# Kernel tuning notes

Hardware: AMD Instinct MI355X
Metric: run time of the kernel (lower is better)

## Reference

```python
import jax, jax.numpy as jnp
import numpy as np

N_HEADS = 4  # from init_kwargs


def setup_inputs() -> dict:
    rng = jax.random.key(0)
    ks = jax.random.split(rng, 7)
    S, B, D = 512, 16, 2048  # seqlen must equal head_dim (D // N_HEADS) per module's reshape
    w_scale = 0.02  # keep logits in a sane range so softmax is not one-hot
    return {
        "query": jax.random.normal(ks[0], (S, B, D), dtype=jnp.float32),
        "key": jax.random.normal(ks[1], (S, B, D), dtype=jnp.float32),
        "value": jax.random.normal(ks[2], (S, B, D), dtype=jnp.float32),
        "Wq": jax.random.normal(ks[3], (D, D), dtype=jnp.float32) * w_scale,
        "Wk": jax.random.normal(ks[4], (D, D), dtype=jnp.float32) * w_scale,
        "Wv": jax.random.normal(ks[5], (D, D), dtype=jnp.float32) * w_scale,
        "Wo": jax.random.normal(ks[6], (D, D), dtype=jnp.float32) * w_scale,
    }


def reference(query, key, value, Wq, Wk, Wv, Wo):
    # Dropout layers act as identity (inference mode). RoPE helper exists in the
    # original module but is never invoked in forward(), so it is omitted.
    S, B, D = query.shape
    H = N_HEADS
    hd = D // H  # head_dim; note S == hd is required by the original reshapes

    def split_heads(x, W):
        # torch Linear: x @ W.T ; then (S,B,D)->(S,B,H,hd)->(H,B,S,hd)->(H*B,S,hd)
        y = x @ W.T
        return y.reshape(S, B, H, hd).transpose(2, 1, 0, 3).reshape(H * B, S, hd)

    q = split_heads(query, Wq)
    k = split_heads(key, Wk)
    v = split_heads(value, Wv)

    scores = jnp.einsum("nsd,ntd->nst", q, k) / jnp.sqrt(jnp.float32(hd))
    attn = jax.nn.softmax(scores, axis=-1)          # (H*B, S, S)
    out = jnp.einsum("nst,ntd->nsd", attn, v)        # (H*B, S, hd)

    # output: (H*B,S,hd)->(H,B,S,hd)->permute(1,2,0,3)->(B,S,H,hd)
    out4 = out.reshape(H, B, S, hd).transpose(1, 2, 0, 3)
    # attn_score reshape relies on S == hd, faithfully reproduced
    attn_score = attn.reshape(H, B, S, hd).transpose(1, 2, 0, 3)  # (B,S,H,hd)

    # .transpose(1,2).contiguous().view(S,B,-1): row-major reinterpret of (B,H,S,hd)
    out4 = jnp.swapaxes(out4, 1, 2)  # (B,H,S,hd)
    output = out4.reshape(S, B, D)

    output = output @ Wo.T
    return output, attn_score
```

## Files before the change

kernel.cpp:

```cpp
#include <hip/hip_runtime.h>
#include <hip/hip_bf16.h>
#include <math.h>

using bf16 = __hip_bfloat16;
typedef __attribute__((ext_vector_type(4))) float f32x4;
typedef __attribute__((ext_vector_type(8))) short s16x8;

#define BM 256
#define BN 256
#define BK 32
#define SLOT 16384
#define BREG 8192

__device__ __forceinline__ short f2b(float f) {
  bf16 h = __float2bfloat16(f);
  short s; __builtin_memcpy(&s, &h, 2); return s;
}

__device__ __forceinline__ void async16(const bf16* g, bf16* l) {
  __builtin_amdgcn_global_load_lds(
      (const __attribute__((address_space(1))) void*)g,
      (__attribute__((address_space(3))) void*)l, 16, 0, 0);
}

__device__ __forceinline__ f32x4 vmax4(f32x4 a, f32x4 b) {
  f32x4 r;
#pragma unroll
  for (int j = 0; j < 4; j++) r[j] = fmaxf(a[j], b[j]);
  return r;
}

template<int MODE, bool CF32>
__global__ __launch_bounds__(512, 2) void gemm_nt(const bf16* __restrict__ Ain,
    const bf16* __restrict__ Bin, void* __restrict__ Cout,
    int K, int lda, int ldb, int ldc, float alpha)
{
  __shared__ bf16 lds[4 * SLOT];

  const int tid  = threadIdx.x;
  const int lane = tid & 63;
  const int wave = tid >> 6;
  const int quad = lane >> 4;
  const int l16  = lane & 15;

  const int nwg = gridDim.x * gridDim.y * gridDim.z;
  int bid = (blockIdx.z * gridDim.y + blockIdx.y) * gridDim.x + blockIdx.x;
  bid = (bid & 7) * (nwg >> 3) + (bid >> 3);
  const int bx = bid % gridDim.x;
  int rest = bid / gridDim.x;
  const int by = rest % gridDim.y;
  const int bz = rest / gridDim.y;

  size_t aBase = 0, bBase = 0, cBase = 0;
  if (MODE == 2) {
    aBase = (size_t)(bz & 15) * 1048576 + (size_t)(bz >> 4) * 512;
    bBase = (size_t)bz * 262144;
    cBase = (size_t)((bz & 15) * 4 + (bz >> 4)) * 262144;
  }

  const int tileM = by * BM;
  const int tileN = bx * BN;

  const int sRow = tid >> 2;
  const int sQ   = (tid & 3) ^ ((tid >> 3) & 3);
  const int sCol = sQ * 8;
  const size_t aOff0 = aBase + (size_t)(tileM + sRow) * lda + sCol;
  const size_t aOff1 = aOff0 + (size_t)128 * lda;
  const size_t bOff0 = bBase + (size_t)(tileN + sRow) * ldb + sCol;
  const size_t bOff1 = bOff0 + (size_t)128 * ldb;
  const int t8 = tid * 8;

  const int warpRow = (wave >> 2) * 128;
  const int warpCol = (wave & 3) * 64;
  int offA[8], offB[4];
#pragma unroll
  for (int mi = 0; mi < 8; mi++) {
    const int R = warpRow + mi * 16 + l16;
    offA[mi] = R * 32 + ((quad ^ ((R >> 1) & 3)) * 8);
  }
#pragma unroll
  for (int ni = 0; ni < 4; ni++) {
    const int R = warpCol + ni * 16 + l16;
    offB[ni] = BREG + R * 32 + ((quad ^ ((R >> 1) & 3)) * 8);
  }

  f32x4 acc[8][4] = {};
  const int NT = K / BK;

#pragma unroll
  for (int p = 0; p < 3; ++p) {
    bf16* base = lds + p * SLOT;
    const int ks = p * BK;
    async16(Ain + aOff0 + ks, base + t8);
    async16(Ain + aOff1 + ks, base + 4096 + t8);
    async16(Bin + bOff0 + ks, base + BREG + t8);
    async16(Bin + bOff1 + ks, base + BREG + 4096 + t8);
  }
  asm volatile("s_waitcnt vmcnt(8)" ::: "memory");
  __builtin_amdgcn_s_barrier();

  for (int g = 0; g < NT; ++g) {
    if (g + 3 < NT) {
      bf16* base = lds + ((g + 3) & 3) * SLOT;
      const int ks = (g + 3) * BK;
      async16(Ain + aOff0 + ks, base + t8);
      async16(Ain + aOff1 + ks, base + 4096 + t8);
      async16(Bin + bOff0 + ks, base + BREG + t8);
      async16(Bin + bOff1 + ks, base + BREG + 4096 + t8);
    }

    const bf16* lb = lds + (g & 3) * SLOT;
    s16x8 af[8], bfr[4];
#pragma unroll
    for (int mi = 0; mi < 8; mi++) af[mi] = *(const s16x8*)(lb + offA[mi]);
#pragma unroll
    for (int ni = 0; ni < 4; ni++) bfr[ni] = *(const s16x8*)(lb + offB[ni]);

    __builtin_amdgcn_s_setprio(1);
#pragma unroll
    for (int mi = 0; mi < 8; mi++)
#pragma unroll
      for (int ni = 0; ni < 4; ni++)
        acc[mi][ni] = __builtin_amdgcn_mfma_f32_16x16x32_bf16(af[mi], bfr[ni], acc[mi][ni], 0, 0, 0);
    __builtin_amdgcn_s_setprio(0);

    if (g < NT - 1) {
      const int ahead = (g + 3 < NT ? 2 : (g + 2 < NT ? NT - 2 - g : 0));
      if (ahead == 2)      asm volatile("s_waitcnt vmcnt(8)" ::: "memory");
      else if (ahead == 1) asm volatile("s_waitcnt vmcnt(4)" ::: "memory");
      else                 asm volatile("s_waitcnt vmcnt(0)" ::: "memory");
      __builtin_amdgcn_s_barrier();
    }
  }

#pragma unroll
  for (int mi = 0; mi < 8; mi++) {
#pragma unroll
    for (int ni = 0; ni < 4; ni++) {
      f32x4 v = acc[mi][ni];
      const int col = tileN + warpCol + ni * 16 + l16;
#pragma unroll
      for (int r = 0; r < 4; r++) {
        const int row = tileM + warpRow + mi * 16 + quad * 4 + r;
        const float val = v[r] * alpha;
        size_t dst;
        if (MODE == 0) {
          dst = (((size_t)((col >> 9) * 16 + (row & 15)) * 512 + (size_t)(row >> 4)) * 512)
                + (size_t)(col & 511);
        } else {
          dst = cBase + (size_t)row * ldc + (size_t)col;
        }
        if (CF32) ((float*)Cout)[dst] = val;
        else      ((bf16*)Cout)[dst] = __float2bfloat16(val);
      }
    }
  }
}

#define SSLOT 20480
__global__ __launch_bounds__(512, 2) void scores_softmax(
    const bf16* __restrict__ Q, const bf16* __restrict__ Kh,
    float* __restrict__ P, bf16* __restrict__ Pb, float alpha)
{
  __shared__ bf16 lds[3 * SSLOT];

  const int tid  = threadIdx.x;
  const int lane = tid & 63;
  const int wave = tid >> 6;
  const int quad = lane >> 4;
  const int l16  = lane & 15;

  int bid = blockIdx.z * 4 + blockIdx.y;
  bid = (bid & 7) * 32 + (bid >> 3);
  const int by = bid & 3;
  const int bz = bid >> 2;

  const size_t aBase = (size_t)bz * 262144;
  const size_t bBase = (size_t)bz * 262144;
  const size_t cBase = (size_t)(bz & 15) * 1048576 + (size_t)(bz >> 4) * 512;
  const int tileM = by * 128;

  const int sRow = tid >> 2;
  const int sQz  = (tid & 3) ^ ((tid >> 3) & 3);
  const int sCol = sQz * 8;
  const size_t aOff = aBase + (size_t)(tileM + sRow) * 512 + sCol;
  const size_t bOff = bBase + (size_t)sRow * 512 + sCol;
  const int t8 = tid * 8;

  const int warpRow = (wave >> 2) * 64;
  const int warpCol = (wave & 3) * 128;
  int offA[4], offB[8];
#pragma unroll
  for (int mi = 0; mi < 4; mi++) {
    const int R = warpRow + mi * 16 + l16;
    offA[mi] = R * 32 + ((quad ^ ((R >> 1) & 3)) * 8);
  }
#pragma unroll
  for (int ni = 0; ni < 8; ni++) {
    const int R = warpCol + ni * 16 + l16;
    offB[ni] = 4096 + R * 32 + ((quad ^ ((R >> 1) & 3)) * 8);
  }

  f32x4 acc[4][8] = {};

#pragma unroll
  for (int p = 0; p < 2; ++p) {
    bf16* base = lds + p * SSLOT;
    const int ks = p * BK;
    async16(Q + aOff + ks, base + t8);
#pragma unroll
    for (int c = 0; c < 4; c++)
      async16(Kh + bOff + c * 65536 + ks, base + 4096 + c * 4096 + t8);
  }
  asm volatile("s_waitcnt vmcnt(5)" ::: "memory");
  __builtin_amdgcn_s_barrier();

  for (int g = 0; g < 16; ++g) {
    if (g + 2 < 16) {
      bf16* base = lds + ((g + 2) % 3) * SSLOT;
      const int ks = (g + 2) * BK;
      async16(Q + aOff + ks, base + t8);
#pragma unroll
      for (int c = 0; c < 4; c++)
        async16(Kh + bOff + c * 65536 + ks, base + 4096 + c * 4096 + t8);
    }

    const bf16* lb = lds + (g % 3) * SSLOT;
    s16x8 af[4], bfr[8];
#pragma unroll
    for (int mi = 0; mi < 4; mi++) af[mi] = *(const s16x8*)(lb + offA[mi]);
#pragma unroll
    for (int ni = 0; ni < 8; ni++) bfr[ni] = *(const s16x8*)(lb + offB[ni]);

    __builtin_amdgcn_s_setprio(1);
#pragma unroll
    for (int mi = 0; mi < 4; mi++)
#pragma unroll
      for (int ni = 0; ni < 8; ni++)
        acc[mi][ni] = __builtin_amdgcn_mfma_f32_16x16x32_bf16(af[mi], bfr[ni], acc[mi][ni], 0, 0, 0);
    __builtin_amdgcn_s_setprio(0);

    if (g + 2 < 16) {
      asm volatile("s_waitcnt vmcnt(5)" ::: "memory");
      __builtin_amdgcn_s_barrier();
    } else if (g + 1 < 16) {
      asm volatile("s_waitcnt vmcnt(0)" ::: "memory");
      __builtin_amdgcn_s_barrier();
    }
  }

  __syncthreads();
  float* red  = (float*)lds;
  float* red2 = red + 512;
  const int wv = wave & 3;

#pragma unroll
  for (int mi = 0; mi < 4; mi++)
#pragma unroll
    for (int ni = 0; ni < 8; ni++) acc[mi][ni] *= alpha;

  f32x4 gm[4];
#pragma unroll
  for (int mi = 0; mi < 4; mi++) {
    f32x4 mx = acc[mi][0];
#pragma unroll
    for (int ni = 1; ni < 8; ni++) mx = vmax4(mx, acc[mi][ni]);
#pragma unroll
    for (int off = 1; off <= 8; off <<= 1) {
      f32x4 o;
#pragma unroll
      for (int r = 0; r < 4; r++) o[r] = __shfl_xor(mx[r], off, 64);
      mx = vmax4(mx, o);
    }
    if (l16 == 0) {
      const int rw = warpRow + mi * 16 + quad * 4;
#pragma unroll
      for (int r = 0; r < 4; r++) red[(rw + r) * 4 + wv] = mx[r];
    }
  }
  __syncthreads();
#pragma unroll
  for (int mi = 0; mi < 4; mi++) {
    const int rw = warpRow + mi * 16 + quad * 4;
#pragma unroll
    for (int r = 0; r < 4; r++) {
      f32x4 p = *(const f32x4*)&red[(rw + r) * 4];
      gm[mi][r] = fmaxf(fmaxf(p[0], p[1]), fmaxf(p[2], p[3]));
    }
  }
  f32x4 sm[4] = {};
#pragma unroll
  for (int mi = 0; mi < 4; mi++)
#pragma unroll
    for (int ni = 0; ni < 8; ni++) {
      f32x4 v = acc[mi][ni];
#pragma unroll
      for (int r = 0; r < 4; r++) v[r] = __expf(v[r] - gm[mi][r]);
      acc[mi][ni] = v;
      sm[mi] += v;
    }
#pragma unroll
  for (int mi = 0; mi < 4; mi++) {
#pragma unroll
    for (int off = 1; off <= 8; off <<= 1) {
      f32x4 o;
#pragma unroll
      for (int r = 0; r < 4; r++) o[r] = __shfl_xor(sm[mi][r], off, 64);
      sm[mi] += o;
    }
    if (l16 == 0) {
      const int rw = warpRow + mi * 16 + quad * 4;
#pragma unroll
      for (int r = 0; r < 4; r++) red2[(rw + r) * 4 + wv] = sm[mi][r];
    }
  }
  __syncthreads();
#pragma unroll
  for (int mi = 0; mi < 4; mi++) {
    const int rw = warpRow + mi * 16 + quad * 4;
#pragma unroll
    for (int r = 0; r < 4; r++) {
      f32x4 p = *(const f32x4*)&red2[(rw + r) * 4];
      gm[mi][r] = 1.f / (p[0] + p[1] + p[2] + p[3]);
    }
  }
#pragma unroll
  for (int mi = 0; mi < 4; mi++)
#pragma unroll
    for (int ni = 0; ni < 8; ni++) {
      const int col = warpCol + ni * 16 + l16;
#pragma unroll
      for (int r = 0; r < 4; r++) {
        const int row = tileM + warpRow + mi * 16 + quad * 4 + r;
        const size_t idx = cBase + (size_t)row * 2048 + col;
        const float val = acc[mi][ni][r] * gm[mi][r];
        P[idx]  = val;
        Pb[idx] = __float2bfloat16(val);
      }
    }
}

struct Conv6 {
  const float* src[6];
  bf16* dst[6];
  int n[6];
};

__global__ __launch_bounds__(256) void convert6(Conv6 a) {
  const int t = blockIdx.y;
  const float* __restrict__ src = a.src[t];
  bf16* __restrict__ dst = a.dst[t];
  const size_t n = (size_t)a.n[t];
  const size_t stride = (size_t)gridDim.x * 256 * 64;
  for (size_t i = ((size_t)blockIdx.x * 256 + threadIdx.x) * 64; i < n; i += stride) {
    f32x4 x[16];
#pragma unroll
    for (int j = 0; j < 16; j++) x[j] = *(const f32x4*)(src + i + j * 4);
    s16x8 r[8];
#pragma unroll
    for (int j = 0; j < 8; j++) {
#pragma unroll
      for (int k = 0; k < 4; k++) {
        r[j][k]     = f2b(x[2 * j][k]);
        r[j][4 + k] = f2b(x[2 * j + 1][k]);
      }
    }
#pragma unroll
    for (int j = 0; j < 8; j++) *(s16x8*)(dst + i + j * 8) = r[j];
  }
}

__global__ __launch_bounds__(256) void transpose512(const bf16* __restrict__ V,
                                                    bf16* __restrict__ VT) {
  __shared__ bf16 tile[32][33];
  const int n = blockIdx.z;
  const bf16* src = V + (size_t)n * 262144;
  bf16* dst = VT + (size_t)n * 262144;
  const int x = blockIdx.x * 32 + threadIdx.x;
#pragma unroll
  for (int i = 0; i < 32; i += 8)
    tile[threadIdx.y + i][threadIdx.x] =
        src[(size_t)(blockIdx.y * 32 + threadIdx.y + i) * 512 + x];
  __syncthreads();
  const int tcol = blockIdx.y * 32 + threadIdx.x;
#pragma unroll
  for (int i = 0; i < 32; i += 8)
    dst[(size_t)(blockIdx.x * 32 + threadIdx.y + i) * 512 + tcol] =
        tile[threadIdx.x][threadIdx.y + i];
}

extern "C" void kernel_launch(void* const* d_in, const int* in_sizes, int n_in,
                              void* d_out, int out_size, void* d_ws, size_t ws_size,
                              hipStream_t stream) {
  const float* query = (const float*)d_in[0];
  const float* key   = (const float*)d_in[1];
  const float* value = (const float*)d_in[2];
  const float* Wq = (const float*)d_in[3];
  const float* Wk = (const float*)d_in[4];
  const float* Wv = (const float*)d_in[5];
  const float* Wo = (const float*)d_in[6];
  float* out = (float*)d_out;
  float* P   = out + 16777216;

  bf16* ws0 = (bf16*)d_ws;
  bf16* ws1 = ws0 + 16777216;
  bf16* o0  = (bf16*)d_out;
  bf16* o1  = o0 + 16777216;
  bf16* p0  = (bf16*)P;
  bf16* p1  = p0 + 16777216;

  const dim3 blk(256);
  const dim3 gblk(512);
  const float inv_sqrt_hd = 0.04419417382415922f;

  Conv6 c;
  c.src[0] = query; c.dst[0] = ws0;           c.n[0] = 16777216;
  c.src[1] = key;   c.dst[1] = ws1;           c.n[1] = 16777216;
  c.src[2] = value; c.dst[2] = p0;            c.n[2] = 16777216;
  c.src[3] = Wq;    c.dst[3] = p1;            c.n[3] = 4194304;
  c.src[4] = Wk;    c.dst[4] = p1 + 4194304;  c.n[4] = 4194304;
  c.src[5] = Wv;    c.dst[5] = p1 + 8388608;  c.n[5] = 4194304;
  convert6<<<dim3(1024, 6), blk, 0, stream>>>(c);

  gemm_nt<0, false><<<dim3(8, 32, 1), gblk, 0, stream>>>(ws0, p1,           o0,  2048, 2048, 2048, 0, 1.0f);
  gemm_nt<0, false><<<dim3(8, 32, 1), gblk, 0, stream>>>(ws1, p1 + 4194304, o1,  2048, 2048, 2048, 0, 1.0f);
  gemm_nt<0, false><<<dim3(8, 32, 1), gblk, 0, stream>>>(p0,  p1 + 8388608, ws0, 2048, 2048, 2048, 0, 1.0f);

  scores_softmax<<<dim3(1, 4, 64), gblk, 0, stream>>>(o0, o1, P, ws1, inv_sqrt_hd);

  transpose512<<<dim3(16, 16, 64), dim3(32, 8), 0, stream>>>(ws0, o0);

  gemm_nt<2, false><<<dim3(2, 2, 64), gblk, 0, stream>>>(ws1, o0, ws0, 512, 2048, 512, 512, 1.0f);

  Conv6 cw;
  for (int i = 0; i < 6; i++) { cw.src[i] = Wo; cw.dst[i] = ws1; cw.n[i] = 4194304; }
  convert6<<<dim3(256, 1), blk, 0, stream>>>(cw);

  gemm_nt<3, true><<<dim3(8, 32, 1), gblk, 0, stream>>>(ws0, ws1, out, 2048, 2048, 2048, 2048, 1.0f);
}
```

Baseline: 711.0 us.

## Rewrite GEMM as 8-wave quadrant-pipelined kernel with BK=64 double buffer

Replaces the 4-stage BK=32 GEMM main loop with a two-slot BK=64 double-buffered scheme. Each wave computes four 64x32 quadrant sub-tiles, and LDS reads, async global-to-LDS staging and MFMA bursts are interleaved with barriers between each quadrant. The aim is to overlap memory traffic with matrix-core work more finely and to cut per-iteration loop overhead. The convert kernel is also changed to a strided coalesced access pattern with an occupancy hint. The many barriers and the tighter waitcnt scheduling risk stalls if the ordering is not balanced.

```diff
diff --git a/kernel.cpp b/kernel.cpp
--- a/kernel.cpp
+++ b/kernel.cpp
@@ -5,12 +5,6 @@
 using bf16 = __hip_bfloat16;
 typedef __attribute__((ext_vector_type(4))) float f32x4;
 typedef __attribute__((ext_vector_type(8))) short s16x8;
-
-#define BM 256
-#define BN 256
-#define BK 32
-#define SLOT 16384
-#define BREG 8192
 
 __device__ __forceinline__ short f2b(float f) {
   bf16 h = __float2bfloat16(f);
@@ -30,12 +24,62 @@
   return r;
 }
 
+#define BAR __builtin_amdgcn_s_barrier()
+#define VM6 asm volatile("s_waitcnt vmcnt(6)" ::: "memory")
+#define VM0 asm volatile("s_waitcnt vmcnt(0)" ::: "memory")
+
+#define STG_A(S, h, tile) do { \
+  const bf16* g_ = aS0 + (size_t)((h) * 128) * lda + (size_t)(tile) * 64; \
+  bf16* d_ = lds + (S) * 32768 + (h) * 8192 + stD; \
+  async16(g_, d_); async16(g_ + (size_t)64 * lda, d_ + 4096); } while (0)
+
+#define STG_B(S, h, tile) do { \
+  const bf16* g_ = bS0 + (size_t)((h) * 128) * ldb + (size_t)(tile) * 64; \
+  bf16* d_ = lds + (S) * 32768 + 16384 + (h) * 8192 + stD; \
+  async16(g_, d_); async16(g_ + (size_t)64 * ldb, d_ + 4096); } while (0)
+
+#define RD_A(S, qm) do { \
+  const bf16* pa0_ = lds + (S) * 32768 + (qm) * 8192 + rdA0; \
+  const bf16* pa1_ = lds + (S) * 32768 + (qm) * 8192 + rdA1; \
+  _Pragma("unroll") for (int mi = 0; mi < 4; mi++) { \
+    af[mi * 2]     = *(const s16x8*)(pa0_ + mi * 1024); \
+    af[mi * 2 + 1] = *(const s16x8*)(pa1_ + mi * 1024); } } while (0)
+
+#define RD_B(S, qn, B) do { \
+  const bf16* pb0_ = lds + (S) * 32768 + 16384 + (qn) * 8192 + rdB0; \
+  const bf16* pb1_ = lds + (S) * 32768 + 16384 + (qn) * 8192 + rdB1; \
+  _Pragma("unroll") for (int ni = 0; ni < 2; ni++) { \
+    B[ni * 2]     = *(const s16x8*)(pb0_ + ni * 1024); \
+    B[ni * 2 + 1] = *(const s16x8*)(pb1_ + ni * 1024); } } while (0)
+
+#define MM(qm, qn, B) do { \
+  __builtin_amdgcn_s_setprio(1); \
+  _Pragma("unroll") for (int mi = 0; mi < 4; mi++) \
+  _Pragma("unroll") for (int ni = 0; ni < 2; ni++) { \
+    acc[qm][qn][mi][ni] = __builtin_amdgcn_mfma_f32_16x16x32_bf16(af[mi*2],   B[ni*2],   acc[qm][qn][mi][ni], 0, 0, 0); \
+    acc[qm][qn][mi][ni] = __builtin_amdgcn_mfma_f32_16x16x32_bf16(af[mi*2+1], B[ni*2+1], acc[qm][qn][mi][ni], 0, 0, 0); } \
+  __builtin_amdgcn_s_setprio(0); } while (0)
+
+#define GROUP(S, OS, st1, stAll, tO, tN) do { \
+  RD_A(S, 0); RD_B(S, 0, bf0); \
+  if (st1) STG_A(OS, 1, tO); \
+  BAR; MM(0, 0, bf0); BAR; \
+  RD_B(S, 1, bf1); \
+  if (stAll) STG_A(S, 0, tN); \
+  BAR; MM(0, 1, bf1); BAR; \
+  RD_A(S, 1); \
+  if (stAll) STG_B(S, 0, tN); \
+  BAR; MM(1, 1, bf1); BAR; \
+  if (stAll) { STG_B(S, 1, tN); VM6; } else { VM0; } \
+  BAR; MM(1, 0, bf0); BAR; \
+} while (0)
+
 template<int MODE, bool CF32>
-__global__ __launch_bounds__(512, 2) void gemm_nt(const bf16* __restrict__ Ain,
+__global__ __launch_bounds__(512, 2) void gemm8(const bf16* __restrict__ Ain,
     const bf16* __restrict__ Bin, void* __restrict__ Cout,
     int K, int lda, int ldb, int ldc, float alpha)
 {
-  __shared__ bf16 lds[4 * SLOT];
+  __shared__ bf16 lds[2 * 32768];
 
   const int tid  = threadIdx.x;
   const int lane = tid & 63;
@@ -58,105 +102,74 @@
     cBase = (size_t)((bz & 15) * 4 + (bz >> 4)) * 262144;
   }
 
-  const int tileM = by * BM;
-  const int tileN = bx * BN;
-
-  const int sRow = tid >> 2;
-  const int sQ   = (tid & 3) ^ ((tid >> 3) & 3);
-  const int sCol = sQ * 8;
-  const size_t aOff0 = aBase + (size_t)(tileM + sRow) * lda + sCol;
-  const size_t aOff1 = aOff0 + (size_t)128 * lda;
-  const size_t bOff0 = bBase + (size_t)(tileN + sRow) * ldb + sCol;
-  const size_t bOff1 = bOff0 + (size_t)128 * ldb;
-  const int t8 = tid * 8;
-
-  const int warpRow = (wave >> 2) * 128;
-  const int warpCol = (wave & 3) * 64;
-  int offA[8], offB[4];
-#pragma unroll
-  for (int mi = 0; mi < 8; mi++) {
-    const int R = warpRow + mi * 16 + l16;
-    offA[mi] = R * 32 + ((quad ^ ((R >> 1) & 3)) * 8);
-  }
-#pragma unroll
-  for (int ni = 0; ni < 4; ni++) {
-    const int R = warpCol + ni * 16 + l16;
-    offB[ni] = BREG + R * 32 + ((quad ^ ((R >> 1) & 3)) * 8);
-  }
-
-  f32x4 acc[8][4] = {};
-  const int NT = K / BK;
-
-#pragma unroll
-  for (int p = 0; p < 3; ++p) {
-    bf16* base = lds + p * SLOT;
-    const int ks = p * BK;
-    async16(Ain + aOff0 + ks, base + t8);
-    async16(Ain + aOff1 + ks, base + 4096 + t8);
-    async16(Bin + bOff0 + ks, base + BREG + t8);
-    async16(Bin + bOff1 + ks, base + BREG + 4096 + t8);
-  }
-  asm volatile("s_waitcnt vmcnt(8)" ::: "memory");
-  __builtin_amdgcn_s_barrier();
-
-  for (int g = 0; g < NT; ++g) {
-    if (g + 3 < NT) {
-      bf16* base = lds + ((g + 3) & 3) * SLOT;
-      const int ks = (g + 3) * BK;
-      async16(Ain + aOff0 + ks, base + t8);
-      async16(Ain + aOff1 + ks, base + 4096 + t8);
-      async16(Bin + bOff0 + ks, base + BREG + t8);
-      async16(Bin + bOff1 + ks, base + BREG + 4096 + t8);
-    }
-
-    const bf16* lb = lds + (g & 3) * SLOT;
-    s16x8 af[8], bfr[4];
-#pragma unroll
-    for (int mi = 0; mi < 8; mi++) af[mi] = *(const s16x8*)(lb + offA[mi]);
-#pragma unroll
-    for (int ni = 0; ni < 4; ni++) bfr[ni] = *(const s16x8*)(lb + offB[ni]);
-
-    __builtin_amdgcn_s_setprio(1);
-#pragma unroll
-    for (int mi = 0; mi < 8; mi++)
-#pragma unroll
-      for (int ni = 0; ni < 4; ni++)
-        acc[mi][ni] = __builtin_amdgcn_mfma_f32_16x16x32_bf16(af[mi], bfr[ni], acc[mi][ni], 0, 0, 0);
-    __builtin_amdgcn_s_setprio(0);
-
-    if (g < NT - 1) {
-      const int ahead = (g + 3 < NT ? 2 : (g + 2 < NT ? NT - 2 - g : 0));
-      if (ahead == 2)      asm volatile("s_waitcnt vmcnt(8)" ::: "memory");
-      else if (ahead == 1) asm volatile("s_waitcnt vmcnt(4)" ::: "memory");
-      else                 asm volatile("s_waitcnt vmcnt(0)" ::: "memory");
-      __builtin_amdgcn_s_barrier();
-    }
-  }
-
-#pragma unroll
-  for (int mi = 0; mi < 8; mi++) {
-#pragma unroll
-    for (int ni = 0; ni < 4; ni++) {
-      f32x4 v = acc[mi][ni];
-      const int col = tileN + warpCol + ni * 16 + l16;
-#pragma unroll
-      for (int r = 0; r < 4; r++) {
-        const int row = tileM + warpRow + mi * 16 + quad * 4 + r;
-        const float val = v[r] * alpha;
-        size_t dst;
-        if (MODE == 0) {
-          dst = (((size_t)((col >> 9) * 16 + (row & 15)) * 512 + (size_t)(row >> 4)) * 512)
-                + (size_t)(col & 511);
-        } else {
-          dst = cBase + (size_t)row * ldc + (size_t)col;
-        }
-        if (CF32) ((float*)Cout)[dst] = val;
-        else      ((bf16*)Cout)[dst] = __float2bfloat16(val);
+  const int tileM = by * 256;
+  const int tileN = bx * 256;
+
+  const int stD = (tid >> 3) * 64 + (tid & 7) * 8;
+  const int sgc = ((tid & 7) ^ ((tid >> 3) & 7)) * 8;
+  const bf16* aS0 = Ain + aBase + (size_t)(tileM + (tid >> 3)) * lda + sgc;
+  const bf16* bS0 = Bin + bBase + (size_t)(tileN + (tid >> 3)) * ldb + sgc;
+
+  const int wrow = (wave >> 2) * 64;
+  const int wcol = (wave & 3) * 32;
+  const int kg08 = (quad ^ (l16 & 7)) * 8;
+  const int rdA0 = (wrow + l16) * 64 + kg08;
+  const int rdA1 = rdA0 ^ 32;
+  const int rdB0 = (wcol + l16) * 64 + kg08;
+  const int rdB1 = rdB0 ^ 32;
+
+  f32x4 acc[2][2][4][2] = {};
+  s16x8 af[8], bf0[4], bf1[4];
+
+  const int NI = K / 128;
+
+  STG_A(0, 0, 0); STG_B(0, 0, 0); STG_B(0, 1, 0); STG_A(0, 1, 0);
+  STG_A(1, 0, 1); STG_B(1, 0, 1); STG_B(1, 1, 1);
+  VM6;
+  BAR;
+
+  for (int it = 0; it < NI; ++it) {
+    const bool sa = (it + 1 < NI);
+    GROUP(0, 1, true, sa, 2 * it + 1, 2 * it + 2);
+    GROUP(1, 0, sa,   sa, 2 * it + 2, 2 * it + 3);
+  }
+
+#pragma unroll
+  for (int qm = 0; qm < 2; qm++)
+#pragma unroll
+  for (int qn = 0; qn < 2; qn++)
+#pragma unroll
+  for (int mi = 0; mi < 4; mi++)
+#pragma unroll
+  for (int ni = 0; ni < 2; ni++) {
+    f32x4 v = acc[qm][qn][mi][ni];
+    const int col = tileN + qn * 128 + wcol + ni * 16 + l16;
+    const int rowb = tileM + qm * 128 + wrow + mi * 16 + quad * 4;
+#pragma unroll
+    for (int r = 0; r < 4; r++) {
+      const int row = rowb + r;
+      const float val = v[r] * alpha;
+      size_t dst;
+      if (MODE == 0) {
+        dst = (((size_t)((col >> 9) * 16 + (row & 15)) * 512 + (size_t)(row >> 4)) * 512)
+              + (size_t)(col & 511);
+      } else {
+        dst = cBase + (size_t)row * ldc + (size_t)col;
       }
-    }
-  }
-}
-
+      if (CF32) ((float*)Cout)[dst] = val;
+      else      ((bf16*)Cout)[dst] = __float2bfloat16(val);
+    }
+  }
+}
+
+#undef GROUP
+#undef MM
+#undef RD_A
+#undef RD_B
+#undef STG_A
+#undef STG_B
+
+#define BK 32
 #define SSLOT 20480
 __global__ __launch_bounds__(512, 2) void scores_softmax(
     const bf16* __restrict__ Q, const bf16* __restrict__ Kh,
@@ -346,27 +359,30 @@
   int n[6];
 };
 
-__global__ __launch_bounds__(256) void convert6(Conv6 a) {
+__global__ __launch_bounds__(256, 4) void convert6(Conv6 a) {
   const int t = blockIdx.y;
   const float* __restrict__ src = a.src[t];
   bf16* __restrict__ dst = a.dst[t];
   const size_t n = (size_t)a.n[t];
-  const size_t stride = (size_t)gridDim.x * 256 * 64;
-  for (size_t i = ((size_t)blockIdx.x * 256 + threadIdx.x) * 64; i < n; i += stride) {
-    f32x4 x[16];
-#pragma unroll
-    for (int j = 0; j < 16; j++) x[j] = *(const f32x4*)(src + i + j * 4);
-    s16x8 r[8];
+  for (size_t base = (size_t)blockIdx.x * 16384; base < n;
+       base += (size_t)gridDim.x * 16384) {
+    const size_t o = base + (size_t)threadIdx.x * 8;
+    f32x4 x[8], y[8];
 #pragma unroll
     for (int j = 0; j < 8; j++) {
+      x[j] = *(const f32x4*)(src + o + j * 2048);
+      y[j] = *(const f32x4*)(src + o + j * 2048 + 4);
+    }
+#pragma unroll
+    for (int j = 0; j < 8; j++) {
+      s16x8 r;
 #pragma unroll
       for (int k = 0; k < 4; k++) {
-        r[j][k]     = f2b(x[2 * j][k]);
-        r[j][4 + k] = f2b(x[2 * j + 1][k]);
+        r[k]     = f2b(x[j][k]);
+        r[4 + k] = f2b(y[j][k]);
       }
-    }
-#pragma unroll
-    for (int j = 0; j < 8; j++) *(s16x8*)(dst + i + j * 8) = r[j];
+      *(s16x8*)(dst + o + j * 2048) = r;
+    }
   }
 }
 
@@ -422,19 +438,19 @@
   c.src[5] = Wv;    c.dst[5] = p1 + 8388608;  c.n[5] = 4194304;
   convert6<<<dim3(1024, 6), blk, 0, stream>>>(c);
 
-  gemm_nt<0, false><<<dim3(8, 32, 1), gblk, 0, stream>>>(ws0, p1,           o0,  2048, 2048, 2048, 0, 1.0f);
-  gemm_nt<0, false><<<dim3(8, 32, 1), gblk, 0, stream>>>(ws1, p1 + 4194304, o1,  2048, 2048, 2048, 0, 1.0f);
-  gemm_nt<0, false><<<dim3(8, 32, 1), gblk, 0, stream>>>(p0,  p1 + 8388608, ws0, 2048, 2048, 2048, 0, 1.0f);
+  gemm8<0, false><<<dim3(8, 32, 1), gblk, 0, stream>>>(ws0, p1,           o0,  2048, 2048, 2048, 0, 1.0f);
+  gemm8<0, false><<<dim3(8, 32, 1), gblk, 0, stream>>>(ws1, p1 + 4194304, o1,  2048, 2048, 2048, 0, 1.0f);
+  gemm8<0, false><<<dim3(8, 32, 1), gblk, 0, stream>>>(p0,  p1 + 8388608, ws0, 2048, 2048, 2048, 0, 1.0f);
 
   scores_softmax<<<dim3(1, 4, 64), gblk, 0, stream>>>(o0, o1, P, ws1, inv_sqrt_hd);
 
   transpose512<<<dim3(16, 16, 64), dim3(32, 8), 0, stream>>>(ws0, o0);
 
-  gemm_nt<2, false><<<dim3(2, 2, 64), gblk, 0, stream>>>(ws1, o0, ws0, 512, 2048, 512, 512, 1.0f);
+  gemm8<2, false><<<dim3(2, 2, 64), gblk, 0, stream>>>(ws1, o0, ws0, 512, 2048, 512, 512, 1.0f);
 
   Conv6 cw;
   for (int i = 0; i < 6; i++) { cw.src[i] = Wo; cw.dst[i] = ws1; cw.n[i] = 4194304; }
   convert6<<<dim3(256, 1), blk, 0, stream>>>(cw);
 
-  gemm_nt<3, true><<<dim3(8, 32, 1), gblk, 0, stream>>>(ws0, ws1, out, 2048, 2048, 2048, 2048, 1.0f);
-}
+  gemm8<3, true><<<dim3(8, 32, 1), gblk, 0, stream>>>(ws0, ws1, out, 2048, 2048, 2048, 2048, 1.0f);
+}
```

Result: faster. 655.1 us (-7.9%).
